# Performance work log

Hardware: AMD Instinct MI355X
Metric: run time of the kernel (lower is better)

The kernel has to match this reference:

```python
import jax, jax.numpy as jnp
import numpy as np

N, E, ENC, EMB, PI = 100000, 1600000, 128, 128, 98
ALPHA1, ALPHA2 = 0.5, 0.5


def setup_inputs() -> dict:
    key = jax.random.key(0)
    ks = jax.random.split(key, 20)
    s = 0.05
    return {
        "x": jax.random.normal(ks[0], (N, ENC), jnp.float32),
        "d2an": jax.random.normal(ks[1], (N, PI), jnp.float32),
        "ei0": jax.random.randint(ks[2], (2, E), 0, N, jnp.int32),
        "ew0": jax.random.uniform(ks[3], (E,), jnp.float32, 0.1, 4.0),
        "ei1": jax.random.randint(ks[4], (2, E), 0, N, jnp.int32),
        "ew1": jax.random.uniform(ks[5], (E,), jnp.float32, 0.1, 4.0),
        "nodeW1": jax.random.normal(ks[6], (ENC, ENC + PI), jnp.float32) * s,
        "nodeW2": jax.random.normal(ks[7], (ENC, ENC + PI), jnp.float32) * s,
        "W1a": jax.random.normal(ks[8], (EMB, ENC), jnp.float32) * s,
        "W1b": jax.random.normal(ks[9], (EMB, ENC), jnp.float32) * s,
        "W2a": jax.random.normal(ks[10], (EMB, ENC), jnp.float32) * s,
        "W2b": jax.random.normal(ks[11], (EMB, ENC), jnp.float32) * s,
        "W3a": jax.random.normal(ks[12], (EMB, EMB), jnp.float32) * s,
        "W3b": jax.random.normal(ks[13], (EMB, EMB), jnp.float32) * s,
        "W4a": jax.random.normal(ks[14], (EMB, EMB), jnp.float32) * s,
        "W4b": jax.random.normal(ks[15], (EMB, EMB), jnp.float32) * s,
    }


def _layer(x, ei, ew, W1, W2, nodeW, d2an, first):
    """PosKnnGNNLayer.forward: add self loops, optional nodeLin, GCN deg norm +
    edge norm, gather -> lin1/lin2 -> scale -> scatter-add (aggr='add')."""
    n = x.shape[0]
    loop = jnp.arange(n, dtype=ei.dtype)
    row = jnp.concatenate([ei[0], loop])          # source nodes (x_j)
    col = jnp.concatenate([ei[1], loop])          # target nodes (aggregation)
    attr = jnp.concatenate([ew, jnp.ones((n,), ew.dtype)])  # self-loop fill=1.0
    if first:
        x = jnp.concatenate([x, d2an], axis=1) @ nodeW.T
    deg = jax.ops.segment_sum(jnp.ones_like(attr), col, num_segments=n)
    dis = jnp.where(deg > 0, jax.lax.rsqrt(jnp.maximum(deg, 1.0)), 0.0)
    deg_norm = dis[row] * dis[col]                # [E']
    einv = attr ** -0.5
    einv = jnp.where(jnp.isinf(einv), 0.0, einv)
    einv = jnp.minimum(einv, 1.0)                 # clamp >1 to 1
    h1 = x @ W1.T                                 # [N, out]
    h2 = x @ W2.T
    msg = deg_norm[:, None] * h1[row] + einv[:, None] * h2[row]  # [E', out]
    return jax.ops.segment_sum(msg, col, num_segments=n)


def reference(x, d2an, ei0, ew0, ei1, ew1, nodeW1, nodeW2,
              W1a, W1b, W2a, W2b, W3a, W3b, W4a, W4b):
    # eval mode: dropout(p=0.3) is identity
    x0 = jax.nn.relu(_layer(x, ei0, ew0, W1a, W1b, nodeW1, d2an, True))
    x1 = jax.nn.relu(_layer(x, ei1, ew1, W2a, W2b, nodeW2, d2an, True))
    xm = ALPHA1 * x0 + ALPHA2 * x1
    x0 = jax.nn.relu(_layer(xm, ei0, ew0, W3a, W3b, None, None, False))
    x1 = jax.nn.relu(_layer(xm, ei1, ew1, W4a, W4b, None, None, False))
    return ALPHA1 * x0 + ALPHA2 * x1
```

## Files before the change

kernel.cpp:

```cpp
#include <hip/hip_runtime.h>
#include <hip/hip_fp16.h>
#include <stdint.h>

#define NN 100000
#define NE 1600000
#define ETOT (NE + NN)
#define EPB 8192
#define NBLK ((NE + EPB - 1) / EPB)
#define NPB 512
#define NBUK ((NN + NPB - 1) / NPB)

typedef __attribute__((ext_vector_type(8))) short bf16x8;
typedef __attribute__((ext_vector_type(4))) float f32x4;
typedef __attribute__((ext_vector_type(4))) unsigned short us4;
typedef unsigned long long ull;

__device__ __forceinline__ float bf2f(unsigned short u) {
    union { unsigned int i; float f; } x; x.i = ((unsigned int)u) << 16; return x.f;
}
__device__ __forceinline__ unsigned short f2bf(float f) {
    union { float f; unsigned int i; } x; x.f = f;
    unsigned int i = x.i;
    return (unsigned short)((i + 0x7FFFu + ((i >> 16) & 1u)) >> 16);
}
__device__ __forceinline__ int packab(float a, float b) {
    unsigned int ua = __half_as_ushort(__float2half_rn(a));
    unsigned int ub = __half_as_ushort(__float2half_rn(b));
    return (int)(ua | (ub << 16));
}
__device__ __forceinline__ float2 unpackab(int p) {
    float a = __half2float(__ushort_as_half((unsigned short)(p & 0xFFFF)));
    float b = __half2float(__ushort_as_half((unsigned short)(((unsigned int)p) >> 16)));
    return make_float2(a, b);
}

__global__ __launch_bounds__(256) void k_cnt(const int* ei0, const int* ei1, int* cntm) {
    __shared__ int h[NBUK];
    const int* col = (blockIdx.y ? ei1 : ei0) + NE;
    for (int i = threadIdx.x; i < NBUK; i += 256) h[i] = 0;
    __syncthreads();
    int base = blockIdx.x * EPB;
    for (int i = 0; i < EPB / 256; i++) {
        int e = base + i * 256 + threadIdx.x;
        if (e < NE) atomicAdd(&h[col[e] >> 9], 1);
    }
    __syncthreads();
    int* out = cntm + ((size_t)blockIdx.y * NBLK + blockIdx.x) * NBUK;
    for (int i = threadIdx.x; i < NBUK; i += 256) out[i] = h[i];
}

__global__ __launch_bounds__(256) void k_btot(const int* cntm, int* bstart, int* btot) {
    __shared__ int s[256];
    int t = threadIdx.x;
    const int* cnt = cntm + (size_t)blockIdx.y * NBLK * NBUK;
    int tot = 0;
    if (t < NBUK)
        for (int blk = 0; blk < NBLK; blk++) tot += cnt[(size_t)blk * NBUK + t];
    s[t] = tot; __syncthreads();
    for (int off = 1; off < 256; off <<= 1) {
        int u = (t >= off) ? s[t - off] : 0;
        __syncthreads(); s[t] += u; __syncthreads();
    }
    if (t < NBUK) {
        bstart[blockIdx.y * NBUK + t] = s[t] - tot;
        btot[blockIdx.y * NBUK + t] = tot;
    }
}

__global__ __launch_bounds__(256) void k_base2(const int* cntm, const int* bstart, int* basem) {
    __shared__ int s[256];
    int b = blockIdx.x;
    const int* cnt = cntm + (size_t)blockIdx.y * NBLK * NBUK;
    int t = threadIdx.x;
    int v = (t < NBLK) ? cnt[(size_t)t * NBUK + b] : 0;
    s[t] = v; __syncthreads();
    for (int off = 1; off < 256; off <<= 1) {
        int u = (t >= off) ? s[t - off] : 0;
        __syncthreads(); s[t] += u; __syncthreads();
    }
    if (t < NBLK)
        basem[((size_t)blockIdx.y * NBLK + t) * NBUK + b] =
            bstart[blockIdx.y * NBUK + b] + (s[t] - v);
}

__global__ __launch_bounds__(256) void k_scat1(const int* ei0, const float* ew0,
                                               const int* ei1, const float* ew1,
                                               const int* basem, int2* st0, int2* st1) {
    __shared__ int lb[NBUK];
    __shared__ int lc[NBUK];
    const int* er = blockIdx.y ? ei1 : ei0;
    const float* ew = blockIdx.y ? ew1 : ew0;
    int2* st = blockIdx.y ? st1 : st0;
    const int* bm = basem + ((size_t)blockIdx.y * NBLK + blockIdx.x) * NBUK;
    for (int i = threadIdx.x; i < NBUK; i += 256) { lb[i] = bm[i]; lc[i] = 0; }
    __syncthreads();
    int base = blockIdx.x * EPB;
    for (int i = 0; i < EPB / 256; i++) {
        int e = base + i * 256 + threadIdx.x;
        if (e >= NE) break;
        int r = er[e];
        int c = er[NE + e];
        float w = ew[e];
        int bkt = c >> 9;
        int rank = atomicAdd(&lc[bkt], 1);
        st[lb[bkt] + rank] = make_int2(r | ((c & 511) << 17), __float_as_int(w));
    }
}

__global__ __launch_bounds__(256) void k_deg(const int* bstart, const int* btot,
                                             const int2* st0, const int2* st1,
                                             int* deg0, int* deg1) {
    __shared__ int h[NPB];
    int b = blockIdx.x;
    const int2* st = blockIdx.y ? st1 : st0;
    int* deg = blockIdx.y ? deg1 : deg0;
    for (int i = threadIdx.x; i < NPB; i += 256) h[i] = 0;
    __syncthreads();
    int s0 = bstart[blockIdx.y * NBUK + b];
    int tot = btot[blockIdx.y * NBUK + b];
    for (int j = s0 + (int)threadIdx.x; j < s0 + tot; j += 256)
        atomicAdd(&h[(st[j].x >> 17) & 511], 1);
    __syncthreads();
    for (int i = threadIdx.x; i < NPB; i += 256) {
        int node = b * NPB + i;
        if (node < NN) deg[node] = h[i] + 1;
    }
}

__global__ void k_scan1(const int* deg0, const int* deg1, int* rp0, int* rp1s, int* bsum) {
    __shared__ int s[256];
    const int* deg = blockIdx.y ? deg1 : deg0;
    int* rp = (blockIdx.y ? rp1s : rp0) + 1;
    int* bs = bsum + blockIdx.y * 128;
    int tid = threadIdx.x;
    int base = blockIdx.x * 1024 + tid * 4;
    int v0 = 0, v1 = 0, v2 = 0, v3 = 0;
    if (base + 0 < NN) v0 = deg[base + 0];
    if (base + 1 < NN) v1 = deg[base + 1];
    if (base + 2 < NN) v2 = deg[base + 2];
    if (base + 3 < NN) v3 = deg[base + 3];
    int sum = v0 + v1 + v2 + v3;
    s[tid] = sum; __syncthreads();
    for (int off = 1; off < 256; off <<= 1) {
        int t = (tid >= off) ? s[tid - off] : 0;
        __syncthreads(); s[tid] += t; __syncthreads();
    }
    int run = s[tid] - sum;
    if (base + 0 < NN) { run += v0; rp[base + 0] = run; }
    if (base + 1 < NN) { run += v1; rp[base + 1] = run; }
    if (base + 2 < NN) { run += v2; rp[base + 2] = run; }
    if (base + 3 < NN) { run += v3; rp[base + 3] = run; }
    if (tid == 255) bs[blockIdx.x] = s[255];
}

__global__ void k_scan2(int* bsum, int nb) {
    __shared__ int s[128];
    int* bs = bsum + blockIdx.x * 128;
    int tid = threadIdx.x;
    int v = (tid < nb) ? bs[tid] : 0;
    s[tid] = v; __syncthreads();
    for (int off = 1; off < 128; off <<= 1) {
        int t = (tid >= off) ? s[tid - off] : 0;
        __syncthreads(); s[tid] += t; __syncthreads();
    }
    if (tid < nb) bs[tid] = s[tid] - v;
}

__global__ void k_scan3(int* rp0, int* rp1s, const int* bsum) {
    int* rowptr = blockIdx.y ? rp1s : rp0;
    int add = bsum[blockIdx.y * 128 + blockIdx.x];
    int tid = threadIdx.x;
    int base = blockIdx.x * 1024 + tid * 4;
    #pragma unroll
    for (int i = 0; i < 4; i++) {
        int idx = base + i;
        if (idx < NN) rowptr[idx + 1] += add;
    }
    if (blockIdx.x == 0 && tid == 0) rowptr[0] = 0;
}

__global__ void k_self(const int* rp0, const int* rp1s, const int* deg0, const int* deg1,
                       int2* eo0, int2* eo1, float* dis0, float* dis1) {
    int i = blockIdx.x * 256 + threadIdx.x;
    if (i >= NN) return;
    const int* rowptr = blockIdx.y ? rp1s : rp0;
    const int* deg = blockIdx.y ? deg1 : deg0;
    int2* eo = blockIdx.y ? eo1 : eo0;
    float* dis = blockIdx.y ? dis1 : dis0;
    int p = rowptr[i];
    float d = (float)deg[i];
    eo[p] = make_int2(i, packab(1.0f / d, 1.0f));
    dis[i] = rsqrtf(d);
}

__global__ __launch_bounds__(256) void k_scat2(const int* rp0, const int* rp1s,
                                               const int* bstart, const int* btot,
                                               const float* dis0, const float* dis1,
                                               const int2* st0, const int2* st1,
                                               int2* eo0, int2* eo1) {
    __shared__ int lcur[NPB];
    __shared__ float ldis[NPB];
    int b = blockIdx.x;
    const int* rowptr = blockIdx.y ? rp1s : rp0;
    const float* dis = blockIdx.y ? dis1 : dis0;
    const int2* st = blockIdx.y ? st1 : st0;
    int2* eo = blockIdx.y ? eo1 : eo0;
    int nstart = b * NPB;
    for (int i = threadIdx.x; i < NPB; i += 256) {
        int node = nstart + i;
        if (node < NN) { lcur[i] = rowptr[node] + 1; ldis[i] = dis[node]; }
    }
    __syncthreads();
    int s0 = bstart[blockIdx.y * NBUK + b];
    int tot = btot[blockIdx.y * NBUK + b];
    for (int j = s0 + (int)threadIdx.x; j < s0 + tot; j += 256) {
        int2 rec = st[j];
        int cl = (rec.x >> 17) & 511;
        int r  = rec.x & 0x1FFFF;
        float w = __int_as_float(rec.y);
        float a = dis[r] * ldis[cl];
        float bb = fminf(rsqrtf(w), 1.0f);
        int pos = atomicAdd(&lcur[cl], 1);
        eo[pos] = make_int2(r, packab(a, bb));
    }
}

__global__ void k_packx(const float* x, const float* d2, unsigned short* Xc) {
    int idx = blockIdx.x * 256 + threadIdx.x;
    if (idx >= NN * 64) return;
    int r = idx >> 6, k4 = (idx & 63) << 2;
    us4 o;
    if (k4 < 128) {
        float4 v = *(const float4*)(x + (size_t)r * 128 + k4);
        o[0] = f2bf(v.x); o[1] = f2bf(v.y); o[2] = f2bf(v.z); o[3] = f2bf(v.w);
    } else {
        #pragma unroll
        for (int i = 0; i < 4; i++) {
            int k = k4 + i;
            float v = (k < 226) ? d2[(size_t)r * 98 + (k - 128)] : 0.f;
            o[i] = f2bf(v);
        }
    }
    *(us4*)(Xc + (size_t)r * 256 + k4) = o;
}

__global__ void k_packw(const float* wn1, const float* wn2,
                        const float* w1a, const float* w1b,
                        const float* w2a, const float* w2b,
                        const float* w3a, const float* w3b,
                        const float* w4a, const float* w4b,
                        unsigned short* Wfnode, unsigned short* WfL) {
    int idx = blockIdx.x * 256 + threadIdx.x;
    if (idx < 65536) {
        int j = idx & 7, lane = (idx >> 3) & 63, ct = (idx >> 9) & 15, ks = idx >> 13;
        int k = ks * 32 + (lane >> 4) * 8 + j;
        int c = ct * 16 + (lane & 15);
        float v = 0.f;
        if (k < 226) v = (c < 128) ? wn1[c * 226 + k] : wn2[(c - 128) * 226 + k];
        Wfnode[idx] = f2bf(v);
    } else if (idx < 196608) {
        int li = idx - 65536;
        int set = li >> 15, r = li & 32767;
        const float* wa = (set == 0) ? w1a : (set == 1) ? w2a : (set == 2) ? w3a : w4a;
        const float* wb = (set == 0) ? w1b : (set == 1) ? w2b : (set == 2) ? w3b : w4b;
        int j = r & 7, lane = (r >> 3) & 63, ct = (r >> 9) & 7, ks = r >> 12;
        int k = ks * 32 + (lane >> 4) * 8 + j;
        int c = ct * 16 + (lane & 15);
        float v = (k < 128) ? wa[c * 128 + k] : wb[c * 128 + (k - 128)];
        WfL[li] = f2bf(v);
    }
}

template <int SRST, int SOFF>
__global__ __launch_bounds__(256) void k_agg(const unsigned short* S,
                                             const int* rowptr, const int2* eg,
                                             unsigned short* G) {
    int c = blockIdx.x * 4 + (threadIdx.x >> 6);
    int lane = threadIdx.x & 63;
    if (c >= NN) return;
    int half = lane >> 5;
    int hl = lane & 31;
    const unsigned short* Sb = S + SOFF + hl * 4;
    float a0 = 0.f, a1 = 0.f, a2 = 0.f, a3 = 0.f;
    float b0 = 0.f, b1 = 0.f, b2 = 0.f, b3 = 0.f;
    int jb = rowptr[c], je = rowptr[c + 1];
    int j = jb;
    for (; j + 16 <= je; j += 16) {
        int2 e[8]; ull u[8];
        #pragma unroll
        for (int i = 0; i < 8; i++) e[i] = eg[j + 2 * i + half];
        #pragma unroll
        for (int i = 0; i < 8; i++)
            u[i] = *(const ull*)(Sb + (size_t)e[i].x * SRST);
        #pragma unroll
        for (int i = 0; i < 8; i++) {
            float2 w = unpackab(e[i].y);
            float x0 = bf2f((unsigned short)(u[i] & 0xFFFF));
            float x1 = bf2f((unsigned short)((u[i] >> 16) & 0xFFFF));
            float x2 = bf2f((unsigned short)((u[i] >> 32) & 0xFFFF));
            float x3 = bf2f((unsigned short)(u[i] >> 48));
            a0 += w.x * x0; a1 += w.x * x1; a2 += w.x * x2; a3 += w.x * x3;
            b0 += w.y * x0; b1 += w.y * x1; b2 += w.y * x2; b3 += w.y * x3;
        }
    }
    for (; j + 4 <= je; j += 4) {
        int2 e[2]; ull u[2];
        #pragma unroll
        for (int i = 0; i < 2; i++) e[i] = eg[j + 2 * i + half];
        #pragma unroll
        for (int i = 0; i < 2; i++)
            u[i] = *(const ull*)(Sb + (size_t)e[i].x * SRST);
        #pragma unroll
        for (int i = 0; i < 2; i++) {
            float2 w = unpackab(e[i].y);
            float x0 = bf2f((unsigned short)(u[i] & 0xFFFF));
            float x1 = bf2f((unsigned short)((u[i] >> 16) & 0xFFFF));
            float x2 = bf2f((unsigned short)((u[i] >> 32) & 0xFFFF));
            float x3 = bf2f((unsigned short)(u[i] >> 48));
            a0 += w.x * x0; a1 += w.x * x1; a2 += w.x * x2; a3 += w.x * x3;
            b0 += w.y * x0; b1 += w.y * x1; b2 += w.y * x2; b3 += w.y * x3;
        }
    }
    for (; j < je; j += 2) {
        int idx = j + half;
        int2 e;
        if (idx < je) e = eg[idx];
        else          e = make_int2(eg[j].x, 0);
        ull u = *(const ull*)(Sb + (size_t)e.x * SRST);
        float2 w = unpackab(e.y);
        float x0 = bf2f((unsigned short)(u & 0xFFFF));
        float x1 = bf2f((unsigned short)((u >> 16) & 0xFFFF));
        float x2 = bf2f((unsigned short)((u >> 32) & 0xFFFF));
        float x3 = bf2f((unsigned short)(u >> 48));
        a0 += w.x * x0; a1 += w.x * x1; a2 += w.x * x2; a3 += w.x * x3;
        b0 += w.y * x0; b1 += w.y * x1; b2 += w.y * x2; b3 += w.y * x3;
    }
    a0 += __shfl_xor(a0, 32); a1 += __shfl_xor(a1, 32);
    a2 += __shfl_xor(a2, 32); a3 += __shfl_xor(a3, 32);
    b0 += __shfl_xor(b0, 32); b1 += __shfl_xor(b1, 32);
    b2 += __shfl_xor(b2, 32); b3 += __shfl_xor(b3, 32);
    unsigned int* gd = (unsigned int*)(G + (size_t)c * 256);
    if (half == 0) {
        gd[2 * hl]     = (unsigned int)f2bf(a0) | ((unsigned int)f2bf(a1) << 16);
        gd[2 * hl + 1] = (unsigned int)f2bf(a2) | ((unsigned int)f2bf(a3) << 16);
    } else {
        gd[64 + 2 * hl]     = (unsigned int)f2bf(b0) | ((unsigned int)f2bf(b1) << 16);
        gd[64 + 2 * hl + 1] = (unsigned int)f2bf(b2) | ((unsigned int)f2bf(b3) << 16);
    }
}

template <int MODE>
__global__ __launch_bounds__(256) void k_gemm(const unsigned short* A, int arst,
                                              const unsigned short* Wf, int nct_total,
                                              unsigned short* outB, float* outF,
                                              const unsigned short* T, int orst) {
    int wave = threadIdx.x >> 6, lane = threadIdx.x & 63;
    int m = lane & 15, quad = lane >> 4;
    int row0 = blockIdx.x * 64 + wave * 16;
    int arow = row0 + m;
    bool rowok = arow < NN;
    const unsigned short* Ap = A + (size_t)arow * arst + quad * 8;
    int ctbase = blockIdx.y * 8;
    f32x4 acc[8];
    #pragma unroll
    for (int t = 0; t < 8; t++) acc[t] = (f32x4){0.f, 0.f, 0.f, 0.f};

    #pragma unroll
    for (int ks = 0; ks < 8; ks++) {
        bf16x8 a;
        if (rowok) a = *(const bf16x8*)(Ap + ks * 32);
        else       a = (bf16x8){0, 0, 0, 0, 0, 0, 0, 0};
        const unsigned short* wp = Wf + ((size_t)(ks * nct_total + ctbase) * 64 + lane) * 8;
        #pragma unroll
        for (int t = 0; t < 8; t++) {
            bf16x8 b = *(const bf16x8*)(wp + t * 512);
            acc[t] = __builtin_amdgcn_mfma_f32_16x16x32_bf16(a, b, acc[t], 0, 0, 0);
        }
    }

    int col0 = blockIdx.y * 128;
    #pragma unroll
    for (int t = 0; t < 8; t++) {
        int c = col0 + t * 16 + m;
        #pragma unroll
        for (int rg = 0; rg < 4; rg++) {
            int r = row0 + quad * 4 + rg;
            if (r < NN) {
                float v = acc[t][rg];
                if (MODE == 0) {
                    outB[(size_t)r * orst + c] = f2bf(v);
                } else {
                    float tv = bf2f(T[(size_t)r * 128 + c]);
                    float o = 0.5f * fmaxf(tv, 0.f) + 0.5f * fmaxf(v, 0.f);
                    if (MODE == 1) outB[(size_t)r * orst + c] = f2bf(o);
                    else           outF[(size_t)r * 128 + c] = o;
                }
            }
        }
    }
}

extern "C" void kernel_launch(void* const* d_in, const int* in_sizes, int n_in,
                              void* d_out, int out_size, void* d_ws, size_t ws_size,
                              hipStream_t stream) {
    const float* x      = (const float*)d_in[0];
    const float* d2an   = (const float*)d_in[1];
    const int*   ei0    = (const int*)d_in[2];
    const float* ew0    = (const float*)d_in[3];
    const int*   ei1    = (const int*)d_in[4];
    const float* ew1    = (const float*)d_in[5];
    const float* nodeW1 = (const float*)d_in[6];
    const float* nodeW2 = (const float*)d_in[7];
    const float* W1a = (const float*)d_in[8],  *W1b = (const float*)d_in[9];
    const float* W2a = (const float*)d_in[10], *W2b = (const float*)d_in[11];
    const float* W3a = (const float*)d_in[12], *W3b = (const float*)d_in[13];
    const float* W4a = (const float*)d_in[14], *W4b = (const float*)d_in[15];
    float* out = (float*)d_out;

    char* p = (char*)d_ws;
    auto alloc = [&](size_t bytes) -> char* {
        char* r = p; p += (bytes + 255) & ~(size_t)255; return r;
    };
    unsigned short* bufA   = (unsigned short*)alloc((size_t)NN * 256 * 2);
    unsigned short* bufB   = (unsigned short*)alloc((size_t)NN * 256 * 2);
    unsigned short* Tbuf   = (unsigned short*)alloc((size_t)NN * 128 * 2);
    unsigned short* Wfnode = (unsigned short*)alloc(65536 * 2);
    unsigned short* WfL    = (unsigned short*)alloc((size_t)4 * 32768 * 2);
    int*    deg0    = (int*)alloc((size_t)NN * 4);
    int*    deg1    = (int*)alloc((size_t)NN * 4);
    int*    rowptr0 = (int*)alloc((size_t)(NN + 1) * 4);
    int*    rowptr1 = (int*)alloc((size_t)(NN + 1) * 4);
    int*    bsum    = (int*)alloc(2 * 128 * 4);
    float*  dis0    = (float*)alloc((size_t)NN * 4);
    float*  dis1    = (float*)alloc((size_t)NN * 4);
    int2*   eo0     = (int2*)alloc((size_t)ETOT * 8);
    int2*   eo1     = (int2*)alloc((size_t)ETOT * 8);
    int*    cntm    = (int*)alloc((size_t)2 * NBLK * NBUK * 4);
    int*    basem   = (int*)alloc((size_t)2 * NBLK * NBUK * 4);
    int*    btot    = (int*)alloc((size_t)2 * NBUK * 4);
    int*    bstart  = (int*)alloc((size_t)2 * NBUK * 4);

    int2* st0 = (int2*)bufB;
    int2* st1 = st0 + NE;

    int nbN  = (NN + 255) / 256;
    int nbS  = (NN + 1023) / 1024;
    dim3 gP((NN + 63) / 64, 2);
    dim3 gL((NN + 63) / 64, 1);
    int nbA = (NN + 3) / 4;

    k_cnt<<<dim3(NBLK, 2), 256, 0, stream>>>(ei0, ei1, cntm);
    k_btot<<<dim3(1, 2), 256, 0, stream>>>(cntm, bstart, btot);
    k_base2<<<dim3(NBUK, 2), 256, 0, stream>>>(cntm, bstart, basem);
    k_scat1<<<dim3(NBLK, 2), 256, 0, stream>>>(ei0, ew0, ei1, ew1, basem, st0, st1);
    k_deg<<<dim3(NBUK, 2), 256, 0, stream>>>(bstart, btot, st0, st1, deg0, deg1);
    k_scan1<<<dim3(nbS, 2), 256, 0, stream>>>(deg0, deg1, rowptr0, rowptr1, bsum);
    k_scan2<<<2, 128, 0, stream>>>(bsum, nbS);
    k_scan3<<<dim3(nbS, 2), 256, 0, stream>>>(rowptr0, rowptr1, bsum);
    k_self<<<dim3(nbN, 2), 256, 0, stream>>>(rowptr0, rowptr1, deg0, deg1,
                                             eo0, eo1, dis0, dis1);
    k_scat2<<<dim3(NBUK, 2), 256, 0, stream>>>(rowptr0, rowptr1, bstart, btot,
                                               dis0, dis1, st0, st1, eo0, eo1);

    k_packx<<<(NN * 64 + 255) / 256, 256, 0, stream>>>(x, d2an, bufA);
    k_packw<<<768, 256, 0, stream>>>(nodeW1, nodeW2, W1a, W1b, W2a, W2b,
                                     W3a, W3b, W4a, W4b, Wfnode, WfL);

    k_gemm<0><<<gP, 256, 0, stream>>>(bufA, 256, Wfnode, 16, bufB, nullptr, nullptr, 256);
    k_agg<256, 0><<<nbA, 256, 0, stream>>>(bufB, rowptr0, eo0, bufA);
    k_gemm<0><<<gL, 256, 0, stream>>>(bufA, 256, WfL, 8, Tbuf, nullptr, nullptr, 128);
    k_agg<256, 128><<<nbA, 256, 0, stream>>>(bufB, rowptr1, eo1, bufA);
    k_gemm<1><<<gL, 256, 0, stream>>>(bufA, 256, WfL + 32768, 8, bufB, nullptr, Tbuf, 128);

    k_agg<128, 0><<<nbA, 256, 0, stream>>>(bufB, rowptr0, eo0, bufA);
    k_gemm<0><<<gL, 256, 0, stream>>>(bufA, 256, WfL + 2 * 32768, 8, Tbuf, nullptr, nullptr, 128);
    k_agg<128, 0><<<nbA, 256, 0, stream>>>(bufB, rowptr1, eo1, bufA);
    k_gemm<2><<<gL, 256, 0, stream>>>(bufA, 256, WfL + 3 * 32768, 8, nullptr, out, Tbuf, 128);
}
```

Before: 778.2 us.

## Fuse CSR build preprocessing kernels and merge pack kernels to cut launches

Merges the bucket-total and per-block base kernels into one serial single-block kernel. Replaces the degree, three-pass scan and self-loop kernels with a per-bucket kernel that computes rowptr locally, because bucket start offsets already give global positions. Combines the x and weight packing kernels into one launch and adds scheduling barriers in the aggregation gather loop to keep loads grouped. This removes several kernel launches and intermediate deg/bsum buffers, but the merged base kernel now walks all blocks serially in one block per graph.

```diff
diff --git a/kernel.cpp b/kernel.cpp
--- a/kernel.cpp
+++ b/kernel.cpp
@@ -9,6 +9,7 @@
 #define NBLK ((NE + EPB - 1) / EPB)
 #define NPB 512
 #define NBUK ((NN + NPB - 1) / NPB)
+#define PACKX_NB ((NN * 64 + 255) / 256)
 
 typedef __attribute__((ext_vector_type(8))) short bf16x8;
 typedef __attribute__((ext_vector_type(4))) float f32x4;
@@ -49,7 +50,8 @@
     for (int i = threadIdx.x; i < NBUK; i += 256) out[i] = h[i];
 }
 
-__global__ __launch_bounds__(256) void k_btot(const int* cntm, int* bstart, int* btot) {
+__global__ __launch_bounds__(256) void k_bases(const int* cntm, int* bstart, int* btot,
+                                               int* basem) {
     __shared__ int s[256];
     int t = threadIdx.x;
     const int* cnt = cntm + (size_t)blockIdx.y * NBLK * NBUK;
@@ -61,26 +63,17 @@
         int u = (t >= off) ? s[t - off] : 0;
         __syncthreads(); s[t] += u; __syncthreads();
     }
+    int bs = s[t] - tot;
     if (t < NBUK) {
-        bstart[blockIdx.y * NBUK + t] = s[t] - tot;
+        bstart[blockIdx.y * NBUK + t] = bs;
         btot[blockIdx.y * NBUK + t] = tot;
-    }
-}
-
-__global__ __launch_bounds__(256) void k_base2(const int* cntm, const int* bstart, int* basem) {
-    __shared__ int s[256];
-    int b = blockIdx.x;
-    const int* cnt = cntm + (size_t)blockIdx.y * NBLK * NBUK;
-    int t = threadIdx.x;
-    int v = (t < NBLK) ? cnt[(size_t)t * NBUK + b] : 0;
-    s[t] = v; __syncthreads();
-    for (int off = 1; off < 256; off <<= 1) {
-        int u = (t >= off) ? s[t - off] : 0;
-        __syncthreads(); s[t] += u; __syncthreads();
-    }
-    if (t < NBLK)
-        basem[((size_t)blockIdx.y * NBLK + t) * NBUK + b] =
-            bstart[blockIdx.y * NBUK + b] + (s[t] - v);
+        int run = bs;
+        int* bm = basem + (size_t)blockIdx.y * NBLK * NBUK + t;
+        for (int blk = 0; blk < NBLK; blk++) {
+            bm[(size_t)blk * NBUK] = run;
+            run += cnt[(size_t)blk * NBUK + t];
+        }
+    }
 }
 
 __global__ __launch_bounds__(256) void k_scat1(const int* ei0, const float* ew0,
@@ -107,90 +100,55 @@
     }
 }
 
-__global__ __launch_bounds__(256) void k_deg(const int* bstart, const int* btot,
-                                             const int2* st0, const int2* st1,
-                                             int* deg0, int* deg1) {
+__global__ __launch_bounds__(256) void k_degdis(const int* bstart, const int* btot,
+                                                const int2* st0, const int2* st1,
+                                                int* rp0, int* rp1s,
+                                                float* dis0, float* dis1,
+                                                int2* eo0, int2* eo1) {
     __shared__ int h[NPB];
+    __shared__ int sc[256];
     int b = blockIdx.x;
+    int tid = threadIdx.x;
     const int2* st = blockIdx.y ? st1 : st0;
-    int* deg = blockIdx.y ? deg1 : deg0;
-    for (int i = threadIdx.x; i < NPB; i += 256) h[i] = 0;
+    int* rowptr = blockIdx.y ? rp1s : rp0;
+    float* dis = blockIdx.y ? dis1 : dis0;
+    int2* eo = blockIdx.y ? eo1 : eo0;
+    for (int i = tid; i < NPB; i += 256) h[i] = 0;
     __syncthreads();
     int s0 = bstart[blockIdx.y * NBUK + b];
     int tot = btot[blockIdx.y * NBUK + b];
-    for (int j = s0 + (int)threadIdx.x; j < s0 + tot; j += 256)
+    for (int j = s0 + tid; j < s0 + tot; j += 256)
         atomicAdd(&h[(st[j].x >> 17) & 511], 1);
     __syncthreads();
-    for (int i = threadIdx.x; i < NPB; i += 256) {
-        int node = b * NPB + i;
-        if (node < NN) deg[node] = h[i] + 1;
-    }
-}
-
-__global__ void k_scan1(const int* deg0, const int* deg1, int* rp0, int* rp1s, int* bsum) {
-    __shared__ int s[256];
-    const int* deg = blockIdx.y ? deg1 : deg0;
-    int* rp = (blockIdx.y ? rp1s : rp0) + 1;
-    int* bs = bsum + blockIdx.y * 128;
-    int tid = threadIdx.x;
-    int base = blockIdx.x * 1024 + tid * 4;
-    int v0 = 0, v1 = 0, v2 = 0, v3 = 0;
-    if (base + 0 < NN) v0 = deg[base + 0];
-    if (base + 1 < NN) v1 = deg[base + 1];
-    if (base + 2 < NN) v2 = deg[base + 2];
-    if (base + 3 < NN) v3 = deg[base + 3];
-    int sum = v0 + v1 + v2 + v3;
-    s[tid] = sum; __syncthreads();
+    int nstart = b * NPB;
+    int nloc = NN - nstart; if (nloc > NPB) nloc = NPB;
+    int v0 = (2 * tid < nloc) ? h[2 * tid] + 1 : 0;
+    int v1 = (2 * tid + 1 < nloc) ? h[2 * tid + 1] + 1 : 0;
+    int sum = v0 + v1;
+    sc[tid] = sum; __syncthreads();
     for (int off = 1; off < 256; off <<= 1) {
-        int t = (tid >= off) ? s[tid - off] : 0;
-        __syncthreads(); s[tid] += t; __syncthreads();
-    }
-    int run = s[tid] - sum;
-    if (base + 0 < NN) { run += v0; rp[base + 0] = run; }
-    if (base + 1 < NN) { run += v1; rp[base + 1] = run; }
-    if (base + 2 < NN) { run += v2; rp[base + 2] = run; }
-    if (base + 3 < NN) { run += v3; rp[base + 3] = run; }
-    if (tid == 255) bs[blockIdx.x] = s[255];
-}
-
-__global__ void k_scan2(int* bsum, int nb) {
-    __shared__ int s[128];
-    int* bs = bsum + blockIdx.x * 128;
-    int tid = threadIdx.x;
-    int v = (tid < nb) ? bs[tid] : 0;
-    s[tid] = v; __syncthreads();
-    for (int off = 1; off < 128; off <<= 1) {
-        int t = (tid >= off) ? s[tid - off] : 0;
-        __syncthreads(); s[tid] += t; __syncthreads();
-    }
-    if (tid < nb) bs[tid] = s[tid] - v;
-}
-
-__global__ void k_scan3(int* rp0, int* rp1s, const int* bsum) {
-    int* rowptr = blockIdx.y ? rp1s : rp0;
-    int add = bsum[blockIdx.y * 128 + blockIdx.x];
-    int tid = threadIdx.x;
-    int base = blockIdx.x * 1024 + tid * 4;
-    #pragma unroll
-    for (int i = 0; i < 4; i++) {
-        int idx = base + i;
-        if (idx < NN) rowptr[idx + 1] += add;
-    }
-    if (blockIdx.x == 0 && tid == 0) rowptr[0] = 0;
-}
-
-__global__ void k_self(const int* rp0, const int* rp1s, const int* deg0, const int* deg1,
-                       int2* eo0, int2* eo1, float* dis0, float* dis1) {
-    int i = blockIdx.x * 256 + threadIdx.x;
-    if (i >= NN) return;
-    const int* rowptr = blockIdx.y ? rp1s : rp0;
-    const int* deg = blockIdx.y ? deg1 : deg0;
-    int2* eo = blockIdx.y ? eo1 : eo0;
-    float* dis = blockIdx.y ? dis1 : dis0;
-    int p = rowptr[i];
-    float d = (float)deg[i];
-    eo[p] = make_int2(i, packab(1.0f / d, 1.0f));
-    dis[i] = rsqrtf(d);
+        int u = (tid >= off) ? sc[tid - off] : 0;
+        __syncthreads(); sc[tid] += u; __syncthreads();
+    }
+    int excl = sc[tid] - sum;
+    int ebase = s0 + nstart;
+    if (2 * tid < nloc) {
+        int node = nstart + 2 * tid;
+        int rp = ebase + excl;
+        rowptr[node] = rp;
+        float d = (float)v0;
+        dis[node] = rsqrtf(d);
+        eo[rp] = make_int2(node, packab(1.0f / d, 1.0f));
+    }
+    if (2 * tid + 1 < nloc) {
+        int node = nstart + 2 * tid + 1;
+        int rp = ebase + excl + v0;
+        rowptr[node] = rp;
+        float d = (float)v1;
+        dis[node] = rsqrtf(d);
+        eo[rp] = make_int2(node, packab(1.0f / d, 1.0f));
+    }
+    if (b == NBUK - 1 && tid == 255) rowptr[NN] = ebase + sc[255];
 }
 
 __global__ __launch_bounds__(256) void k_scat2(const int* rp0, const int* rp1s,
@@ -225,32 +183,33 @@
     }
 }
 
-__global__ void k_packx(const float* x, const float* d2, unsigned short* Xc) {
-    int idx = blockIdx.x * 256 + threadIdx.x;
-    if (idx >= NN * 64) return;
-    int r = idx >> 6, k4 = (idx & 63) << 2;
-    us4 o;
-    if (k4 < 128) {
-        float4 v = *(const float4*)(x + (size_t)r * 128 + k4);
-        o[0] = f2bf(v.x); o[1] = f2bf(v.y); o[2] = f2bf(v.z); o[3] = f2bf(v.w);
-    } else {
-        #pragma unroll
-        for (int i = 0; i < 4; i++) {
-            int k = k4 + i;
-            float v = (k < 226) ? d2[(size_t)r * 98 + (k - 128)] : 0.f;
-            o[i] = f2bf(v);
-        }
-    }
-    *(us4*)(Xc + (size_t)r * 256 + k4) = o;
-}
-
-__global__ void k_packw(const float* wn1, const float* wn2,
-                        const float* w1a, const float* w1b,
-                        const float* w2a, const float* w2b,
-                        const float* w3a, const float* w3b,
-                        const float* w4a, const float* w4b,
-                        unsigned short* Wfnode, unsigned short* WfL) {
-    int idx = blockIdx.x * 256 + threadIdx.x;
+__global__ void k_pack(const float* x, const float* d2, unsigned short* Xc,
+                       const float* wn1, const float* wn2,
+                       const float* w1a, const float* w1b,
+                       const float* w2a, const float* w2b,
+                       const float* w3a, const float* w3b,
+                       const float* w4a, const float* w4b,
+                       unsigned short* Wfnode, unsigned short* WfL) {
+    if (blockIdx.x < PACKX_NB) {
+        int idx = blockIdx.x * 256 + threadIdx.x;
+        if (idx >= NN * 64) return;
+        int r = idx >> 6, k4 = (idx & 63) << 2;
+        us4 o;
+        if (k4 < 128) {
+            float4 v = *(const float4*)(x + (size_t)r * 128 + k4);
+            o[0] = f2bf(v.x); o[1] = f2bf(v.y); o[2] = f2bf(v.z); o[3] = f2bf(v.w);
+        } else {
+            #pragma unroll
+            for (int i = 0; i < 4; i++) {
+                int k = k4 + i;
+                float v = (k < 226) ? d2[(size_t)r * 98 + (k - 128)] : 0.f;
+                o[i] = f2bf(v);
+            }
+        }
+        *(us4*)(Xc + (size_t)r * 256 + k4) = o;
+        return;
+    }
+    int idx = (blockIdx.x - PACKX_NB) * 256 + threadIdx.x;
     if (idx < 65536) {
         int j = idx & 7, lane = (idx >> 3) & 63, ct = (idx >> 9) & 15, ks = idx >> 13;
         int k = ks * 32 + (lane >> 4) * 8 + j;
@@ -292,6 +251,7 @@
         #pragma unroll
         for (int i = 0; i < 8; i++)
             u[i] = *(const ull*)(Sb + (size_t)e[i].x * SRST);
+        __builtin_amdgcn_sched_barrier(0);
         #pragma unroll
         for (int i = 0; i < 8; i++) {
             float2 w = unpackab(e[i].y);
@@ -310,6 +270,7 @@
         #pragma unroll
         for (int i = 0; i < 2; i++)
             u[i] = *(const ull*)(Sb + (size_t)e[i].x * SRST);
+        __builtin_amdgcn_sched_barrier(0);
         #pragma unroll
         for (int i = 0; i < 2; i++) {
             float2 w = unpackab(e[i].y);
@@ -426,11 +387,8 @@
     unsigned short* Tbuf   = (unsigned short*)alloc((size_t)NN * 128 * 2);
     unsigned short* Wfnode = (unsigned short*)alloc(65536 * 2);
     unsigned short* WfL    = (unsigned short*)alloc((size_t)4 * 32768 * 2);
-    int*    deg0    = (int*)alloc((size_t)NN * 4);
-    int*    deg1    = (int*)alloc((size_t)NN * 4);
     int*    rowptr0 = (int*)alloc((size_t)(NN + 1) * 4);
     int*    rowptr1 = (int*)alloc((size_t)(NN + 1) * 4);
-    int*    bsum    = (int*)alloc(2 * 128 * 4);
     float*  dis0    = (float*)alloc((size_t)NN * 4);
     float*  dis1    = (float*)alloc((size_t)NN * 4);
     int2*   eo0     = (int2*)alloc((size_t)ETOT * 8);
@@ -443,28 +401,21 @@
     int2* st0 = (int2*)bufB;
     int2* st1 = st0 + NE;
 
-    int nbN  = (NN + 255) / 256;
-    int nbS  = (NN + 1023) / 1024;
     dim3 gP((NN + 63) / 64, 2);
     dim3 gL((NN + 63) / 64, 1);
     int nbA = (NN + 3) / 4;
 
     k_cnt<<<dim3(NBLK, 2), 256, 0, stream>>>(ei0, ei1, cntm);
-    k_btot<<<dim3(1, 2), 256, 0, stream>>>(cntm, bstart, btot);
-    k_base2<<<dim3(NBUK, 2), 256, 0, stream>>>(cntm, bstart, basem);
+    k_bases<<<dim3(1, 2), 256, 0, stream>>>(cntm, bstart, btot, basem);
     k_scat1<<<dim3(NBLK, 2), 256, 0, stream>>>(ei0, ew0, ei1, ew1, basem, st0, st1);
-    k_deg<<<dim3(NBUK, 2), 256, 0, stream>>>(bstart, btot, st0, st1, deg0, deg1);
-    k_scan1<<<dim3(nbS, 2), 256, 0, stream>>>(deg0, deg1, rowptr0, rowptr1, bsum);
-    k_scan2<<<2, 128, 0, stream>>>(bsum, nbS);
-    k_scan3<<<dim3(nbS, 2), 256, 0, stream>>>(rowptr0, rowptr1, bsum);
-    k_self<<<dim3(nbN, 2), 256, 0, stream>>>(rowptr0, rowptr1, deg0, deg1,
-                                             eo0, eo1, dis0, dis1);
+    k_degdis<<<dim3(NBUK, 2), 256, 0, stream>>>(bstart, btot, st0, st1,
+                                                rowptr0, rowptr1, dis0, dis1, eo0, eo1);
     k_scat2<<<dim3(NBUK, 2), 256, 0, stream>>>(rowptr0, rowptr1, bstart, btot,
                                                dis0, dis1, st0, st1, eo0, eo1);
 
-    k_packx<<<(NN * 64 + 255) / 256, 256, 0, stream>>>(x, d2an, bufA);
-    k_packw<<<768, 256, 0, stream>>>(nodeW1, nodeW2, W1a, W1b, W2a, W2b,
-                                     W3a, W3b, W4a, W4b, Wfnode, WfL);
+    k_pack<<<PACKX_NB + 768, 256, 0, stream>>>(x, d2an, bufA,
+                                               nodeW1, nodeW2, W1a, W1b, W2a, W2b,
+                                               W3a, W3b, W4a, W4b, Wfnode, WfL);
 
     k_gemm<0><<<gP, 256, 0, stream>>>(bufA, 256, Wfnode, 16, bufB, nullptr, nullptr, 256);
     k_agg<256, 0><<<nbA, 256, 0, stream>>>(bufB, rowptr0, eo0, bufA);
```

Measured after the change: 784.5 us. About the same (+0.8%).
